# Kernel optimization log

Hardware: AMD Instinct MI355X
Metric: run time of the kernel (lower is better)

Reference implementation:

```python
import jax, jax.numpy as jnp
import numpy as np

NUM_HEADS = 16


def setup_inputs() -> dict:
    key = jax.random.key(0)
    ks = jax.random.split(key, 9)
    B, S, D = 2, 2048, 2048
    s = 1.0 / np.sqrt(D)
    return {
        "x": jax.random.normal(ks[0], (B, S, D), jnp.float32),
        "Wq": jax.random.normal(ks[1], (D, D), jnp.float32) * s,
        "bq": jax.random.normal(ks[2], (D,), jnp.float32) * 0.01,
        "Wk": jax.random.normal(ks[3], (D, D), jnp.float32) * s,
        "bk": jax.random.normal(ks[4], (D,), jnp.float32) * 0.01,
        "Wv": jax.random.normal(ks[5], (D, D), jnp.float32) * s,
        "bv": jax.random.normal(ks[6], (D,), jnp.float32) * 0.01,
        "Wo": jax.random.normal(ks[7], (D, D), jnp.float32) * s,
        "bo": jax.random.normal(ks[8], (D,), jnp.float32) * 0.01,
    }


def reference(x, Wq, bq, Wk, bk, Wv, bv, Wo, bo):
    B, S, D = x.shape
    H = NUM_HEADS
    dh = D // H
    # torch Linear: y = x @ W.T + b
    def proj(W, b):
        return (x @ W.T + b).reshape(B, S, H, dh).transpose(0, 2, 1, 3)  # [B,H,S,dh]
    Q = proj(Wq, bq)
    K = proj(Wk, bk)
    V = proj(Wv, bv)
    scores = jnp.einsum('bhqd,bhkd->bhqk', Q, K) / jnp.sqrt(jnp.float32(dh))
    causal = jnp.tril(jnp.ones((S, S), dtype=bool))  # allow k <= q
    scores = jnp.where(causal, scores, -jnp.inf)
    attn = jax.nn.softmax(scores, axis=-1)
    out = jnp.einsum('bhqk,bhkd->bhqd', attn, V)
    out = out.transpose(0, 2, 1, 3).reshape(B, S, D)
    return out @ Wo.T + bo
```

## Files before the change

### kernel.cpp

```cpp
#include <hip/hip_runtime.h>
#include <hip/hip_bf16.h>

#define B_  2
#define S_  2048
#define D_  2048
#define H_  16
#define DH_ 128
#define M_  (B_*S_)

typedef __hip_bfloat16 bf16;
typedef float v4f __attribute__((ext_vector_type(4)));
typedef short v8s __attribute__((ext_vector_type(8)));

__device__ __forceinline__ short f2s(float x) {
  bf16 h = __float2bfloat16(x);
  return *reinterpret_cast<const short*>(&h);
}
__device__ __forceinline__ v8s ld8(const float* p) {
  v4f a = *reinterpret_cast<const v4f*>(p);
  v4f b = *reinterpret_cast<const v4f*>(p + 4);
  v8s r = { f2s(a[0]), f2s(a[1]), f2s(a[2]), f2s(a[3]),
            f2s(b[0]), f2s(b[1]), f2s(b[2]), f2s(b[3]) };
  return r;
}
__device__ __forceinline__ v8s ld8(const bf16* p) {
  return *reinterpret_cast<const v8s*>(p);
}
__device__ __forceinline__ void store_out(bf16* p, float v)  { *p = __float2bfloat16(v); }
__device__ __forceinline__ void store_out(float* p, float v) { *p = v; }

__device__ __forceinline__ void gll16(const bf16* g, bf16* l) {
  __builtin_amdgcn_global_load_lds((const __attribute__((address_space(1))) void*)g,
                                   (__attribute__((address_space(3))) void*)l,
                                   16, 0, 0);
}

__global__ __launch_bounds__(256) void cvt_f32_bf16(const float* __restrict__ in,
                                                    bf16* __restrict__ out, int n8) {
  int i = blockIdx.x * 256 + threadIdx.x;
  if (i >= n8) return;
  *reinterpret_cast<v8s*>(out + (size_t)i * 8) = ld8(in + (size_t)i * 8);
}

template <int MODE, typename TOUT>
__global__ __launch_bounds__(256) void gemm_bt(const bf16* __restrict__ A,
                                               const bf16* __restrict__ W,
                                               const float* __restrict__ bias,
                                               TOUT* __restrict__ out) {
  __shared__ __align__(16) bf16 As[128 * 32];
  __shared__ __align__(16) bf16 Bs[128 * 32];
  const int tid  = threadIdx.x;
  const int lane = tid & 63, wave = tid >> 6;
  const int wm = wave >> 1, wn = wave & 1;
  const int quad = lane >> 4, l16 = lane & 15;
  const int bm = blockIdx.y * 128, bn = blockIdx.x * 128;

  const bf16* aptr = A + (size_t)(bm + (tid >> 2)) * D_ + (tid & 3) * 8;
  const bf16* bptr = W + (size_t)(bn + (tid >> 2)) * D_ + (tid & 3) * 8;
  bf16* lA0 = As + wave * 512;
  bf16* lA1 = As + 2048 + wave * 512;
  bf16* lB0 = Bs + wave * 512;
  bf16* lB1 = Bs + 2048 + wave * 512;

  v4f acc[4][4] = {};
  for (int k0 = 0; k0 < D_; k0 += 32) {
    gll16(aptr + k0,                    lA0);
    gll16(aptr + (size_t)64 * D_ + k0,  lA1);
    gll16(bptr + k0,                    lB0);
    gll16(bptr + (size_t)64 * D_ + k0,  lB1);
    __syncthreads();
    v8s af[4], bfr[4];
#pragma unroll
    for (int mi = 0; mi < 4; ++mi)
      af[mi] = *reinterpret_cast<const v8s*>(&As[(wm * 64 + mi * 16 + l16) * 32 + quad * 8]);
#pragma unroll
    for (int ni = 0; ni < 4; ++ni)
      bfr[ni] = *reinterpret_cast<const v8s*>(&Bs[(wn * 64 + ni * 16 + l16) * 32 + quad * 8]);
#pragma unroll
    for (int mi = 0; mi < 4; ++mi)
#pragma unroll
      for (int ni = 0; ni < 4; ++ni)
        acc[mi][ni] = __builtin_amdgcn_mfma_f32_16x16x32_bf16(af[mi], bfr[ni], acc[mi][ni], 0, 0, 0);
    __syncthreads();
  }

  constexpr float QSCALE = 0.12752003912f;
#pragma unroll
  for (int ni = 0; ni < 4; ++ni) {
    const int n = bn + wn * 64 + ni * 16 + l16;
    const float bv = bias[n];
#pragma unroll
    for (int mi = 0; mi < 4; ++mi) {
      const int m0 = bm + wm * 64 + mi * 16 + quad * 4;
#pragma unroll
      for (int r = 0; r < 4; ++r) {
        const int m = m0 + r;
        float v = acc[mi][ni][r] + bv;
        size_t idx;
        if (MODE == 0 || MODE == 1) {
          if (MODE == 0) v *= QSCALE;
          int b = m >> 11, s = m & (S_ - 1);
          int h = n >> 7,  d = n & (DH_ - 1);
          idx = ((size_t)(b * H_ + h) * S_ + s) * DH_ + d;
        } else if (MODE == 2) {
          int b = m >> 11, s = m & (S_ - 1);
          int h = n >> 7,  d = n & (DH_ - 1);
          idx = ((size_t)(b * H_ + h) * DH_ + d) * S_ + s;
        } else {
          idx = (size_t)m * D_ + n;
        }
        store_out(out + idx, v);
      }
    }
  }
}

#define QBLK 128
__global__ __launch_bounds__(512, 4) void attn_fused(const bf16* __restrict__ Q,
                                                     const bf16* __restrict__ K,
                                                     const bf16* __restrict__ Vt,
                                                     bf16* __restrict__ Oa) {
  __shared__ __align__(16) bf16 Ks[64 * 128];
  __shared__ __align__(16) bf16 Vs[128 * 64];
  __shared__ __align__(16) bf16 Ps[8][16 * 72];
  const int tid  = threadIdx.x;
  const int lane = tid & 63, wave = tid >> 6;
  const int quad = lane >> 4, l16 = lane & 15;
  const int swz  = l16 & 7;
  const int qt = (int)gridDim.x - 1 - (int)blockIdx.x;
  const int bh = blockIdx.y;
  const int b = bh >> 4, h = bh & 15;
  const bf16* Qh = Q  + (size_t)bh * S_ * DH_;
  const bf16* Kh = K  + (size_t)bh * S_ * DH_;
  const bf16* Vh = Vt + (size_t)bh * DH_ * S_;

  const int qrow0 = qt * QBLK + wave * 16;
  v8s qf[4];
#pragma unroll
  for (int kk = 0; kk < 4; ++kk)
    qf[kk] = *reinterpret_cast<const v8s*>(&Qh[(size_t)(qrow0 + l16) * DH_ + kk * 32 + quad * 8]);

  v4f acc_o[8] = {};
  float m_i[4], l_i[4];
#pragma unroll
  for (int r = 0; r < 4; ++r) { m_i[r] = -1.0e30f; l_i[r] = 0.f; }

  const int nkt = 2 * qt + 2;
  for (int kt = 0; kt < nkt; ++kt) {
    const int kbase = kt * 64;
#pragma unroll
    for (int rr = 0; rr < 2; ++rr) {
      const int g = rr * 512 + tid;
      const int krow = g >> 4, kc = g & 15;
      gll16(Kh + (size_t)(kbase + krow) * DH_ + ((kc ^ (krow & 7)) << 3),
            Ks + rr * 4096 + wave * 512);
      const int vrow = g >> 3, vc = g & 7;
      gll16(Vh + (size_t)vrow * S_ + kbase + ((vc ^ (vrow & 7)) << 3),
            Vs + rr * 4096 + wave * 512);
    }
    __syncthreads();

    const bool active = (kbase <= qrow0 + 15);
    if (active) {
      v4f sc[4];
      __builtin_amdgcn_s_setprio(1);
#pragma unroll
      for (int nt = 0; nt < 4; ++nt) {
        v4f a = {};
#pragma unroll
        for (int kk = 0; kk < 4; ++kk) {
          v8s kf = *reinterpret_cast<const v8s*>(
              &Ks[(nt * 16 + l16) * 128 + (((kk * 4 + quad) ^ swz) << 3)]);
          a = __builtin_amdgcn_mfma_f32_16x16x32_bf16(qf[kk], kf, a, 0, 0, 0);
        }
        sc[nt] = a;
      }
      __builtin_amdgcn_s_setprio(0);
      if (kbase + 63 > qrow0) {
#pragma unroll
        for (int nt = 0; nt < 4; ++nt)
#pragma unroll
          for (int r = 0; r < 4; ++r) {
            int kc2 = kbase + nt * 16 + l16;
            int qr = qrow0 + quad * 4 + r;
            if (kc2 > qr) sc[nt][r] = -1.0e30f;
          }
      }
#pragma unroll
      for (int r = 0; r < 4; ++r) {
        float mx = fmaxf(fmaxf(sc[0][r], sc[1][r]), fmaxf(sc[2][r], sc[3][r]));
        mx = fmaxf(mx, __shfl_xor(mx, 1));
        mx = fmaxf(mx, __shfl_xor(mx, 2));
        mx = fmaxf(mx, __shfl_xor(mx, 4));
        mx = fmaxf(mx, __shfl_xor(mx, 8));
        if (mx > m_i[r] + 8.0f) {
          float alpha = exp2f(m_i[r] - mx);
          m_i[r] = mx;
          l_i[r] *= alpha;
#pragma unroll
          for (int nt8 = 0; nt8 < 8; ++nt8) acc_o[nt8][r] *= alpha;
        }
        const float mm = m_i[r];
        float s0 = exp2f(sc[0][r] - mm);
        float s1 = exp2f(sc[1][r] - mm);
        float s2 = exp2f(sc[2][r] - mm);
        float s3 = exp2f(sc[3][r] - mm);
        sc[0][r] = s0; sc[1][r] = s1; sc[2][r] = s2; sc[3][r] = s3;
        float t = s0 + s1 + s2 + s3;
        t += __shfl_xor(t, 1); t += __shfl_xor(t, 2);
        t += __shfl_xor(t, 4); t += __shfl_xor(t, 8);
        l_i[r] += t;
      }
#pragma unroll
      for (int nt = 0; nt < 4; ++nt)
#pragma unroll
        for (int r = 0; r < 4; ++r)
          Ps[wave][(quad * 4 + r) * 72 + nt * 16 + l16] = __float2bfloat16(sc[nt][r]);
      asm volatile("s_waitcnt lgkmcnt(0)" ::: "memory");
      __builtin_amdgcn_s_setprio(1);
#pragma unroll
      for (int kk2 = 0; kk2 < 2; ++kk2) {
        v8s pf = *reinterpret_cast<const v8s*>(&Ps[wave][l16 * 72 + kk2 * 32 + quad * 8]);
#pragma unroll
        for (int nt8 = 0; nt8 < 8; ++nt8) {
          v8s vf = *reinterpret_cast<const v8s*>(
              &Vs[(nt8 * 16 + l16) * 64 + (((kk2 * 4 + quad) ^ swz) << 3)]);
          acc_o[nt8] = __builtin_amdgcn_mfma_f32_16x16x32_bf16(pf, vf, acc_o[nt8], 0, 0, 0);
        }
      }
      __builtin_amdgcn_s_setprio(0);
    }
    __syncthreads();
  }

#pragma unroll
  for (int r = 0; r < 4; ++r) {
    const float inv = 1.0f / l_i[r];
    const int srow = qrow0 + quad * 4 + r;
#pragma unroll
    for (int nt8 = 0; nt8 < 8; ++nt8)
      Oa[((size_t)b * S_ + srow) * D_ + h * DH_ + nt8 * 16 + l16] =
          __float2bfloat16(acc_o[nt8][r] * inv);
  }
}

extern "C" void kernel_launch(void* const* d_in, const int* in_sizes, int n_in,
                              void* d_out, int out_size, void* d_ws, size_t ws_size,
                              hipStream_t stream) {
  if (n_in != 9 ||
      in_sizes[0] != M_ * D_ ||
      in_sizes[1] != D_ * D_ || in_sizes[2] != D_ ||
      in_sizes[3] != D_ * D_ || in_sizes[4] != D_ ||
      in_sizes[5] != D_ * D_ || in_sizes[6] != D_ ||
      in_sizes[7] != D_ * D_ || in_sizes[8] != D_ ||
      out_size != M_ * D_)
    return;

  const float* x  = (const float*)d_in[0];
  const float* Wq = (const float*)d_in[1];
  const float* bq = (const float*)d_in[2];
  const float* Wk = (const float*)d_in[3];
  const float* bk = (const float*)d_in[4];
  const float* Wv = (const float*)d_in[5];
  const float* bv = (const float*)d_in[6];
  const float* Wo = (const float*)d_in[7];
  const float* bo = (const float*)d_in[8];
  float* out = (float*)d_out;

  const size_t NT = (size_t)M_ * D_;
  bf16* qws   = (bf16*)d_out;
  bf16* xbf   = (bf16*)d_out + NT;
  bf16* kws   = (bf16*)d_ws;
  bf16* vtw   = kws + NT;
  bf16* aws   = vtw + NT;
  bf16* wslot = aws;
  bf16* wo_s  = kws;

  const int N8X = M_ * D_ / 8;
  const int N8W = D_ * D_ / 8;

  dim3 gg(D_ / 128, M_ / 128), bb(256);

  cvt_f32_bf16<<<N8X / 256, bb, 0, stream>>>(x, xbf, N8X);

  cvt_f32_bf16<<<N8W / 256, bb, 0, stream>>>(Wq, wslot, N8W);
  gemm_bt<0, bf16><<<gg, bb, 0, stream>>>(xbf, wslot, bq, qws);

  cvt_f32_bf16<<<N8W / 256, bb, 0, stream>>>(Wk, wslot, N8W);
  gemm_bt<1, bf16><<<gg, bb, 0, stream>>>(xbf, wslot, bk, kws);

  cvt_f32_bf16<<<N8W / 256, bb, 0, stream>>>(Wv, wslot, N8W);
  gemm_bt<2, bf16><<<gg, bb, 0, stream>>>(xbf, wslot, bv, vtw);

  attn_fused<<<dim3(S_ / QBLK, B_ * H_), dim3(512), 0, stream>>>(qws, kws, vtw, aws);

  cvt_f32_bf16<<<N8W / 256, bb, 0, stream>>>(Wo, wo_s, N8W);
  gemm_bt<3, float><<<gg, bb, 0, stream>>>(aws, wo_s, bo, out);
}
```

Baseline: 475.3 us.

## Fuse Q and K projections into one GEMM and drop LDS staging in attention

Q and K weights are converted into one contiguous buffer so a single wider GEMM launch produces both projections, removing one launch and letting the grid fill more CUs. The attention kernel no longer stages K and V tiles in shared memory with block barriers. Each wave now reads K and V fragments straight from global memory and iterates only over its own causal range. Occupancy bounds are lowered. This removes the sync and wasted-iteration overhead but relies on cache for K/V reuse across the waves of a block, with more global traffic and non-coalesced reads.

```diff
diff --git a/kernel.cpp b/kernel.cpp
--- a/kernel.cpp
+++ b/kernel.cpp
@@ -23,9 +23,6 @@
             f2s(b[0]), f2s(b[1]), f2s(b[2]), f2s(b[3]) };
   return r;
 }
-__device__ __forceinline__ v8s ld8(const bf16* p) {
-  return *reinterpret_cast<const v8s*>(p);
-}
 __device__ __forceinline__ void store_out(bf16* p, float v)  { *p = __float2bfloat16(v); }
 __device__ __forceinline__ void store_out(float* p, float v) { *p = v; }
 
@@ -45,8 +42,10 @@
 template <int MODE, typename TOUT>
 __global__ __launch_bounds__(256) void gemm_bt(const bf16* __restrict__ A,
                                                const bf16* __restrict__ W,
-                                               const float* __restrict__ bias,
-                                               TOUT* __restrict__ out) {
+                                               const float* __restrict__ bias0,
+                                               const float* __restrict__ bias1,
+                                               TOUT* __restrict__ out0,
+                                               TOUT* __restrict__ out1) {
   __shared__ __align__(16) bf16 As[128 * 32];
   __shared__ __align__(16) bf16 Bs[128 * 32];
   const int tid  = threadIdx.x;
@@ -85,10 +84,14 @@
   }
 
   constexpr float QSCALE = 0.12752003912f;
+  const int proj = (MODE == 0) ? (bn >> 11) : 0;
+  const float* bias = proj ? bias1 : bias0;
+  TOUT* outp = proj ? out1 : out0;
+  const int bnl = bn & 2047;
 #pragma unroll
   for (int ni = 0; ni < 4; ++ni) {
-    const int n = bn + wn * 64 + ni * 16 + l16;
-    const float bv = bias[n];
+    const int nl = bnl + wn * 64 + ni * 16 + l16;
+    const float bv = bias[nl];
 #pragma unroll
     for (int mi = 0; mi < 4; ++mi) {
       const int m0 = bm + wm * 64 + mi * 16 + quad * 4;
@@ -97,36 +100,33 @@
         const int m = m0 + r;
         float v = acc[mi][ni][r] + bv;
         size_t idx;
-        if (MODE == 0 || MODE == 1) {
-          if (MODE == 0) v *= QSCALE;
+        if (MODE == 0) {
+          if (!proj) v *= QSCALE;
           int b = m >> 11, s = m & (S_ - 1);
-          int h = n >> 7,  d = n & (DH_ - 1);
+          int h = nl >> 7, d = nl & (DH_ - 1);
           idx = ((size_t)(b * H_ + h) * S_ + s) * DH_ + d;
         } else if (MODE == 2) {
           int b = m >> 11, s = m & (S_ - 1);
-          int h = n >> 7,  d = n & (DH_ - 1);
+          int h = nl >> 7, d = nl & (DH_ - 1);
           idx = ((size_t)(b * H_ + h) * DH_ + d) * S_ + s;
         } else {
-          idx = (size_t)m * D_ + n;
+          idx = (size_t)m * D_ + nl;
         }
-        store_out(out + idx, v);
+        store_out(outp + idx, v);
       }
     }
   }
 }
 
 #define QBLK 128
-__global__ __launch_bounds__(512, 4) void attn_fused(const bf16* __restrict__ Q,
+__global__ __launch_bounds__(512, 2) void attn_fused(const bf16* __restrict__ Q,
                                                      const bf16* __restrict__ K,
                                                      const bf16* __restrict__ Vt,
                                                      bf16* __restrict__ Oa) {
-  __shared__ __align__(16) bf16 Ks[64 * 128];
-  __shared__ __align__(16) bf16 Vs[128 * 64];
   __shared__ __align__(16) bf16 Ps[8][16 * 72];
   const int tid  = threadIdx.x;
   const int lane = tid & 63, wave = tid >> 6;
   const int quad = lane >> 4, l16 = lane & 15;
-  const int swz  = l16 & 7;
   const int qt = (int)gridDim.x - 1 - (int)blockIdx.x;
   const int bh = blockIdx.y;
   const int b = bh >> 4, h = bh & 15;
@@ -145,92 +145,76 @@
 #pragma unroll
   for (int r = 0; r < 4; ++r) { m_i[r] = -1.0e30f; l_i[r] = 0.f; }
 
-  const int nkt = 2 * qt + 2;
-  for (int kt = 0; kt < nkt; ++kt) {
+  const int ktend = ((qrow0 + 15) >> 6) + 1;
+  for (int kt = 0; kt < ktend; ++kt) {
     const int kbase = kt * 64;
-#pragma unroll
-    for (int rr = 0; rr < 2; ++rr) {
-      const int g = rr * 512 + tid;
-      const int krow = g >> 4, kc = g & 15;
-      gll16(Kh + (size_t)(kbase + krow) * DH_ + ((kc ^ (krow & 7)) << 3),
-            Ks + rr * 4096 + wave * 512);
-      const int vrow = g >> 3, vc = g & 7;
-      gll16(Vh + (size_t)vrow * S_ + kbase + ((vc ^ (vrow & 7)) << 3),
-            Vs + rr * 4096 + wave * 512);
-    }
-    __syncthreads();
-
-    const bool active = (kbase <= qrow0 + 15);
-    if (active) {
-      v4f sc[4];
-      __builtin_amdgcn_s_setprio(1);
-#pragma unroll
-      for (int nt = 0; nt < 4; ++nt) {
-        v4f a = {};
-#pragma unroll
-        for (int kk = 0; kk < 4; ++kk) {
-          v8s kf = *reinterpret_cast<const v8s*>(
-              &Ks[(nt * 16 + l16) * 128 + (((kk * 4 + quad) ^ swz) << 3)]);
-          a = __builtin_amdgcn_mfma_f32_16x16x32_bf16(qf[kk], kf, a, 0, 0, 0);
+    v4f sc[4];
+    __builtin_amdgcn_s_setprio(1);
+#pragma unroll
+    for (int nt = 0; nt < 4; ++nt) {
+      v4f a = {};
+#pragma unroll
+      for (int kk = 0; kk < 4; ++kk) {
+        v8s kf = *reinterpret_cast<const v8s*>(
+            &Kh[(size_t)(kbase + nt * 16 + l16) * DH_ + (kk * 4 + quad) * 8]);
+        a = __builtin_amdgcn_mfma_f32_16x16x32_bf16(qf[kk], kf, a, 0, 0, 0);
+      }
+      sc[nt] = a;
+    }
+    __builtin_amdgcn_s_setprio(0);
+    if (kbase + 63 > qrow0) {
+#pragma unroll
+      for (int nt = 0; nt < 4; ++nt)
+#pragma unroll
+        for (int r = 0; r < 4; ++r) {
+          int kc2 = kbase + nt * 16 + l16;
+          int qr = qrow0 + quad * 4 + r;
+          if (kc2 > qr) sc[nt][r] = -1.0e30f;
         }
-        sc[nt] = a;
-      }
-      __builtin_amdgcn_s_setprio(0);
-      if (kbase + 63 > qrow0) {
-#pragma unroll
-        for (int nt = 0; nt < 4; ++nt)
-#pragma unroll
-          for (int r = 0; r < 4; ++r) {
-            int kc2 = kbase + nt * 16 + l16;
-            int qr = qrow0 + quad * 4 + r;
-            if (kc2 > qr) sc[nt][r] = -1.0e30f;
-          }
-      }
-#pragma unroll
-      for (int r = 0; r < 4; ++r) {
-        float mx = fmaxf(fmaxf(sc[0][r], sc[1][r]), fmaxf(sc[2][r], sc[3][r]));
-        mx = fmaxf(mx, __shfl_xor(mx, 1));
-        mx = fmaxf(mx, __shfl_xor(mx, 2));
-        mx = fmaxf(mx, __shfl_xor(mx, 4));
-        mx = fmaxf(mx, __shfl_xor(mx, 8));
-        if (mx > m_i[r] + 8.0f) {
-          float alpha = exp2f(m_i[r] - mx);
-          m_i[r] = mx;
-          l_i[r] *= alpha;
-#pragma unroll
-          for (int nt8 = 0; nt8 < 8; ++nt8) acc_o[nt8][r] *= alpha;
-        }
-        const float mm = m_i[r];
-        float s0 = exp2f(sc[0][r] - mm);
-        float s1 = exp2f(sc[1][r] - mm);
-        float s2 = exp2f(sc[2][r] - mm);
-        float s3 = exp2f(sc[3][r] - mm);
-        sc[0][r] = s0; sc[1][r] = s1; sc[2][r] = s2; sc[3][r] = s3;
-        float t = s0 + s1 + s2 + s3;
-        t += __shfl_xor(t, 1); t += __shfl_xor(t, 2);
-        t += __shfl_xor(t, 4); t += __shfl_xor(t, 8);
-        l_i[r] += t;
-      }
-#pragma unroll
-      for (int nt = 0; nt < 4; ++nt)
-#pragma unroll
-        for (int r = 0; r < 4; ++r)
-          Ps[wave][(quad * 4 + r) * 72 + nt * 16 + l16] = __float2bfloat16(sc[nt][r]);
-      asm volatile("s_waitcnt lgkmcnt(0)" ::: "memory");
-      __builtin_amdgcn_s_setprio(1);
-#pragma unroll
-      for (int kk2 = 0; kk2 < 2; ++kk2) {
-        v8s pf = *reinterpret_cast<const v8s*>(&Ps[wave][l16 * 72 + kk2 * 32 + quad * 8]);
-#pragma unroll
-        for (int nt8 = 0; nt8 < 8; ++nt8) {
-          v8s vf = *reinterpret_cast<const v8s*>(
-              &Vs[(nt8 * 16 + l16) * 64 + (((kk2 * 4 + quad) ^ swz) << 3)]);
-          acc_o[nt8] = __builtin_amdgcn_mfma_f32_16x16x32_bf16(pf, vf, acc_o[nt8], 0, 0, 0);
-        }
-      }
-      __builtin_amdgcn_s_setprio(0);
-    }
-    __syncthreads();
+    }
+#pragma unroll
+    for (int r = 0; r < 4; ++r) {
+      float mx = fmaxf(fmaxf(sc[0][r], sc[1][r]), fmaxf(sc[2][r], sc[3][r]));
+      mx = fmaxf(mx, __shfl_xor(mx, 1));
+      mx = fmaxf(mx, __shfl_xor(mx, 2));
+      mx = fmaxf(mx, __shfl_xor(mx, 4));
+      mx = fmaxf(mx, __shfl_xor(mx, 8));
+      if (mx > m_i[r] + 8.0f) {
+        float alpha = exp2f(m_i[r] - mx);
+        m_i[r] = mx;
+        l_i[r] *= alpha;
+#pragma unroll
+        for (int nt8 = 0; nt8 < 8; ++nt8) acc_o[nt8][r] *= alpha;
+      }
+      const float mm = m_i[r];
+      float s0 = exp2f(sc[0][r] - mm);
+      float s1 = exp2f(sc[1][r] - mm);
+      float s2 = exp2f(sc[2][r] - mm);
+      float s3 = exp2f(sc[3][r] - mm);
+      sc[0][r] = s0; sc[1][r] = s1; sc[2][r] = s2; sc[3][r] = s3;
+      float t = s0 + s1 + s2 + s3;
+      t += __shfl_xor(t, 1); t += __shfl_xor(t, 2);
+      t += __shfl_xor(t, 4); t += __shfl_xor(t, 8);
+      l_i[r] += t;
+    }
+#pragma unroll
+    for (int nt = 0; nt < 4; ++nt)
+#pragma unroll
+      for (int r = 0; r < 4; ++r)
+        Ps[wave][(quad * 4 + r) * 72 + nt * 16 + l16] = __float2bfloat16(sc[nt][r]);
+    asm volatile("s_waitcnt lgkmcnt(0)" ::: "memory");
+    __builtin_amdgcn_s_setprio(1);
+#pragma unroll
+    for (int kk2 = 0; kk2 < 2; ++kk2) {
+      v8s pf = *reinterpret_cast<const v8s*>(&Ps[wave][l16 * 72 + kk2 * 32 + quad * 8]);
+#pragma unroll
+      for (int nt8 = 0; nt8 < 8; ++nt8) {
+        v8s vf = *reinterpret_cast<const v8s*>(
+            &Vh[(size_t)(nt8 * 16 + l16) * S_ + kbase + (kk2 * 4 + quad) * 8]);
+        acc_o[nt8] = __builtin_amdgcn_mfma_f32_16x16x32_bf16(pf, vf, acc_o[nt8], 0, 0, 0);
+      }
+    }
+    __builtin_amdgcn_s_setprio(0);
   }
 
 #pragma unroll
@@ -268,32 +252,31 @@
   float* out = (float*)d_out;
 
   const size_t NT = (size_t)M_ * D_;
+  const size_t WN = (size_t)D_ * D_;
   bf16* qws   = (bf16*)d_out;
   bf16* xbf   = (bf16*)d_out + NT;
   bf16* kws   = (bf16*)d_ws;
   bf16* vtw   = kws + NT;
   bf16* aws   = vtw + NT;
-  bf16* wslot = aws;
+  bf16* wqk   = aws;
+  bf16* wv_s  = aws;
   bf16* wo_s  = kws;
 
   const int N8X = M_ * D_ / 8;
   const int N8W = D_ * D_ / 8;
 
-  dim3 gg(D_ / 128, M_ / 128), bb(256);
-
+  dim3 bb(256);
   cvt_f32_bf16<<<N8X / 256, bb, 0, stream>>>(x, xbf, N8X);
-
-  cvt_f32_bf16<<<N8W / 256, bb, 0, stream>>>(Wq, wslot, N8W);
-  gemm_bt<0, bf16><<<gg, bb, 0, stream>>>(xbf, wslot, bq, qws);
-
-  cvt_f32_bf16<<<N8W / 256, bb, 0, stream>>>(Wk, wslot, N8W);
-  gemm_bt<1, bf16><<<gg, bb, 0, stream>>>(xbf, wslot, bk, kws);
-
-  cvt_f32_bf16<<<N8W / 256, bb, 0, stream>>>(Wv, wslot, N8W);
-  gemm_bt<2, bf16><<<gg, bb, 0, stream>>>(xbf, wslot, bv, vtw);
+  cvt_f32_bf16<<<N8W / 256, bb, 0, stream>>>(Wq, wqk, N8W);
+  cvt_f32_bf16<<<N8W / 256, bb, 0, stream>>>(Wk, wqk + WN, N8W);
+
+  gemm_bt<0, bf16><<<dim3(32, 32), bb, 0, stream>>>(xbf, wqk, bq, bk, qws, kws);
+
+  cvt_f32_bf16<<<N8W / 256, bb, 0, stream>>>(Wv, wv_s, N8W);
+  gemm_bt<2, bf16><<<dim3(16, 32), bb, 0, stream>>>(xbf, wv_s, bv, bv, vtw, vtw);
 
   attn_fused<<<dim3(S_ / QBLK, B_ * H_), dim3(512), 0, stream>>>(qws, kws, vtw, aws);
 
   cvt_f32_bf16<<<N8W / 256, bb, 0, stream>>>(Wo, wo_s, N8W);
-  gemm_bt<3, float><<<gg, bb, 0, stream>>>(aws, wo_s, bo, out);
-}
+  gemm_bt<3, float><<<dim3(16, 32), bb, 0, stream>>>(aws, wo_s, bo, bo, out, out);
+}
```

Result: slower. 803.5 us (+69.0%).
